# Optimization experiments

Hardware: AMD Instinct MI355X
Metric: run time of the kernel (lower is better)

## Reference

```python
import jax, jax.numpy as jnp
import numpy as np

B, X, Y, Z, C = 1, 16, 16, 16, 768
NUM_HEADS = 12


def setup_inputs() -> dict:
    key = jax.random.key(0)
    k0, k1, k2 = jax.random.split(key, 3)
    x = jax.random.normal(k0, (B, X, Y, Z, C), dtype=jnp.float32)
    # Linear weights stored as [in, out] (torch stores [out, in]; math is x @ W_in_out + b)
    w_qkv = jax.random.normal(k1, (C, 3 * C), dtype=jnp.float32) * 0.02
    b_qkv = jnp.zeros((3 * C,), dtype=jnp.float32)
    w_proj = jax.random.normal(k2, (C, C), dtype=jnp.float32) * 0.02
    b_proj = jnp.zeros((C,), dtype=jnp.float32)
    return {"x": x, "w_qkv": w_qkv, "b_qkv": b_qkv, "w_proj": w_proj, "b_proj": b_proj}


def reference(x, w_qkv, b_qkv, w_proj, b_proj):
    b, xx, yy, zz, c = x.shape
    h = NUM_HEADS
    hd = c // h
    scale = hd ** (-0.5)
    n = xx * yy * zz  # flatten 3D grid into tokens

    qkv = x.reshape(b, n, c) @ w_qkv + b_qkv          # [B, N, 3C]
    qkv = qkv.reshape(b, n, 3, h, hd).transpose(2, 0, 3, 1, 4)  # [3, B, H, N, hd]
    q, k, v = qkv[0], qkv[1], qkv[2]

    attn = jnp.einsum('bhnd,bhmd->bhnm', q * scale, k)  # [B, H, N, N]
    attn = jax.nn.softmax(attn, axis=-1)
    out = jnp.einsum('bhnm,bhmd->bhnd', attn, v)        # [B, H, N, hd]
    out = out.transpose(0, 2, 1, 3).reshape(b, n, c)
    out = out @ w_proj + b_proj
    return out.reshape(b, xx, yy, zz, c)
```

## Files before the change

### kernel.cpp

```cpp
#include <hip/hip_runtime.h>
#include <cstddef>

#define N_TOK 4096
#define C_DIM 768
#define H_NUM 12
#define C3    2304
#define NSPLIT 4

typedef unsigned short u16;
using short8  = __attribute__((ext_vector_type(8))) short;
using floatx4 = __attribute__((ext_vector_type(4))) float;
using u16x4   = __attribute__((ext_vector_type(4))) u16;
using uint4v  = __attribute__((ext_vector_type(4))) unsigned;

#define K2SCALE 0.18033688011112043f

__device__ __forceinline__ u16 f2bf(float f) {
  union { float f; unsigned u; } v; v.f = f;
  unsigned r = v.u + 0x7FFFu + ((v.u >> 16) & 1u);
  return (u16)(r >> 16);
}

__device__ __forceinline__ unsigned permpack(float a, float b) {
  union { float f; unsigned u; } x, y; x.f = a; y.f = b;
  return __builtin_amdgcn_perm(y.u, x.u, 0x07060302u);
}

__device__ __forceinline__ float aexp2(float x) {
  float r;
  asm("v_exp_f32 %0, %1" : "=v"(r) : "v"(x));
  return r;
}

__device__ __forceinline__ float arcp(float x) {
  float r;
  asm("v_rcp_f32 %0, %1" : "=v"(r) : "v"(x));
  return r;
}

__device__ __forceinline__ void pl_swap32(unsigned &a, unsigned &b) {
#if __has_builtin(__builtin_amdgcn_permlane32_swap)
  auto r = __builtin_amdgcn_permlane32_swap(a, b, false, false);
  a = r[0]; b = r[1];
#else
  asm("v_permlane32_swap_b32 %0, %1" : "+v"(a), "+v"(b));
#endif
}
__device__ __forceinline__ void pl_swap16(unsigned &a, unsigned &b) {
#if __has_builtin(__builtin_amdgcn_permlane16_swap)
  auto r = __builtin_amdgcn_permlane16_swap(a, b, false, false);
  a = r[0]; b = r[1];
#else
  asm("v_permlane16_swap_b32 %0, %1" : "+v"(a), "+v"(b));
#endif
}

__device__ __forceinline__ void gload_lds16(const void* g, void* l) {
  __builtin_amdgcn_global_load_lds(
      (const __attribute__((address_space(1))) unsigned int*)g,
      (__attribute__((address_space(3))) unsigned int*)l, 16, 0, 0);
}

__global__ void k_pre(const float* __restrict__ x, u16* __restrict__ xb,
                      const float* __restrict__ wq, u16* __restrict__ wqT,
                      const float* __restrict__ wp, u16* __restrict__ wpT,
                      float* __restrict__ Oz) {
  __shared__ float tile[32][33];
  const int b = blockIdx.x;
  if (b >= 5376) {
    size_t i = (size_t)(b - 5376) * 256 + threadIdx.x;
    float4 z; z.x = 0.f; z.y = 0.f; z.z = 0.f; z.w = 0.f;
    ((float4*)Oz)[i] = z;
    return;
  }
  if (b < 3072) {
    int i = b * 256 + threadIdx.x;
    float4 f = ((const float4*)x)[i];
    u16x4 o;
    o[0] = f2bf(f.x); o[1] = f2bf(f.y); o[2] = f2bf(f.z); o[3] = f2bf(f.w);
    ((u16x4*)xb)[i] = o;
    return;
  }
  const float* in; u16* out; int Cc, bx, by;
  if (b < 4800) { int t = b - 3072; in = wq; out = wqT; Cc = 2304; bx = t % 72; by = t / 72; }
  else          { int t = b - 4800; in = wp; out = wpT; Cc = 768;  bx = t % 24; by = t / 24; }
  const int R = 768;
  const int tx = threadIdx.x & 31;
  const int ty = threadIdx.x >> 5;
  const int c0 = bx * 32, r0 = by * 32;
#pragma unroll
  for (int i = 0; i < 32; i += 8)
    tile[ty + i][tx] = in[(size_t)(r0 + ty + i) * Cc + c0 + tx];
  __syncthreads();
#pragma unroll
  for (int i = 0; i < 32; i += 8)
    out[(size_t)(c0 + ty + i) * R + r0 + tx] = f2bf(tile[tx][ty + i]);
}

template <int MODE>
__global__ __launch_bounds__(256)
void k_gemm_bt(const u16* __restrict__ A, const u16* __restrict__ B,
               const float* __restrict__ bias, void* __restrict__ outp,
               u16* __restrict__ vT, int K) {
  __shared__ u16 As[2][128 * 32];
  __shared__ u16 Bs[2][128 * 32];
  const int tid  = threadIdx.x;
  const int wave = tid >> 6, lane = tid & 63, quad = lane >> 4, l16 = lane & 15;
  const int wrow = wave >> 1, wcol = wave & 1;
  const int bm = blockIdx.y, bn = blockIdx.x;
  const int r3 = l16 & 3;

  floatx4 acc[4][4];
#pragma unroll
  for (int i = 0; i < 4; ++i)
#pragma unroll
    for (int j = 0; j < 4; ++j)
#pragma unroll
      for (int r = 0; r < 4; ++r) acc[i][j][r] = 0.f;

  const int ar = tid >> 2;
  const int ac = ((tid & 3) ^ (ar & 3)) * 8;
  const u16* gA = A + (size_t)(bm * 128 + ar) * K + ac;
  const u16* gB = B + (size_t)(bn * 128 + ar) * K + ac;

  auto stage = [&](int b, int k0) {
    gload_lds16(gA + k0,                  &As[b][tid * 8]);
    gload_lds16(gA + k0 + (size_t)64 * K, &As[b][tid * 8 + 2048]);
    gload_lds16(gB + k0,                  &Bs[b][tid * 8]);
    gload_lds16(gB + k0 + (size_t)64 * K, &Bs[b][tid * 8 + 2048]);
  };

  stage(0, 0);
  __syncthreads();
  int buf = 0;
  for (int k0 = 0; k0 < K; k0 += 32) {
    if (k0 + 32 < K) stage(buf ^ 1, k0 + 32);
    short8 af[4], bf[4];
#pragma unroll
    for (int t = 0; t < 4; ++t) {
      af[t] = *(const short8*)&As[buf][(wrow * 64 + t * 16 + l16) * 32 + ((quad ^ r3) * 8)];
      bf[t] = *(const short8*)&Bs[buf][(wcol * 64 + t * 16 + l16) * 32 + ((quad ^ r3) * 8)];
    }
#pragma unroll
    for (int tm = 0; tm < 4; ++tm)
#pragma unroll
      for (int tn = 0; tn < 4; ++tn)
        acc[tm][tn] = __builtin_amdgcn_mfma_f32_16x16x32_bf16(af[tm], bf[tn], acc[tm][tn], 0, 0, 0);
    __syncthreads();
    buf ^= 1;
  }

  if (MODE == 0) {
    u16* qkv = (u16*)outp;
    const float qs = (bn < 6) ? K2SCALE : 1.0f;
#pragma unroll
    for (int tn = 0; tn < 4; ++tn) {
      const int col = bn * 128 + wcol * 64 + tn * 16 + l16;
      const float bc = bias[col];
      if (col < 1536) {
#pragma unroll
        for (int tm = 0; tm < 4; ++tm) {
          const int rowb = bm * 128 + wrow * 64 + tm * 16 + quad * 4;
#pragma unroll
          for (int r = 0; r < 4; ++r)
            qkv[(size_t)(rowb + r) * C3 + col] = f2bf((acc[tm][tn][r] + bc) * qs);
        }
      } else {
        const int hd_ = col - 1536;
#pragma unroll
        for (int tm = 0; tm < 4; ++tm) {
          const int rowb = bm * 128 + wrow * 64 + tm * 16 + quad * 4;
          u16x4 pk;
#pragma unroll
          for (int r = 0; r < 4; ++r) pk[r] = f2bf(acc[tm][tn][r] + bc);
          *(u16x4*)&vT[(size_t)hd_ * N_TOK + rowb] = pk;
        }
      }
    }
  } else {
    float* out = (float*)outp;
#pragma unroll
    for (int tn = 0; tn < 4; ++tn) {
      const int col = bn * 128 + wcol * 64 + tn * 16 + l16;
      const float bc = bias[col];
#pragma unroll
      for (int tm = 0; tm < 4; ++tm) {
        const int rowb = bm * 128 + wrow * 64 + tm * 16 + quad * 4;
#pragma unroll
        for (int r = 0; r < 4; ++r)
          out[(size_t)(rowb + r) * C_DIM + col] = acc[tm][tn][r] + bc;
      }
    }
  }
}

__global__ __launch_bounds__(256, 4)
void k_flash(const u16* __restrict__ qkv, const u16* __restrict__ vT,
             float* __restrict__ Opart, float* __restrict__ lpart) {
  __shared__ u16 Ks[2][64 * 64];
  __shared__ u16 Vs[2][64 * 64];
  const int tid  = threadIdx.x;
  const int wave = tid >> 6, lane = tid & 63, quad = lane >> 4, l16 = lane & 15;
  const int h = blockIdx.x >> 2, split = blockIdx.x & 3, qt = blockIdx.y;
  const int lr = tid >> 3;
  const int lc = ((tid & 7) ^ (lr & 7)) * 8;
  const int r7 = l16 & 7;
  const int kb = split * 1024;

  short8 bq[2][2];
#pragma unroll
  for (int qs = 0; qs < 2; ++qs)
#pragma unroll
    for (int ks = 0; ks < 2; ++ks)
      bq[qs][ks] = *(const short8*)&qkv[(size_t)(qt * 128 + wave * 32 + qs * 16 + l16) * C3
                                        + h * 64 + ks * 32 + quad * 8];

  const u16* gk = qkv + (size_t)lr * C3 + C_DIM + h * 64 + lc;
  const u16* gv = vT + (size_t)(h * 64 + lr) * N_TOK + lc;

  auto stage = [&](int b, int m0) {
#pragma unroll
    for (int p = 0; p < 2; ++p) {
      gload_lds16(gk + (size_t)(m0 + p * 32) * C3,    &Ks[b][p * 2048 + tid * 8]);
      gload_lds16(gv + (size_t)(p * 32) * N_TOK + m0, &Vs[b][p * 2048 + tid * 8]);
    }
  };

  floatx4 o0[4], o1[4], l0, l1, zv;
#pragma unroll
  for (int r = 0; r < 4; ++r) { zv[r] = 0.f; l0[r] = 0.f; l1[r] = 0.f; }
#pragma unroll
  for (int d = 0; d < 4; ++d)
#pragma unroll
    for (int r = 0; r < 4; ++r) { o0[d][r] = 0.f; o1[d][r] = 0.f; }

  short8 ones;
#pragma unroll
  for (int i = 0; i < 8; ++i) ones[i] = (short)0x3F80;

  auto compute = [&](int b) __attribute__((always_inline)) {
    const u16* kbp = &Ks[b][0];
    const u16* vb  = &Vs[b][0];
    floatx4 s0[4], s1[4];
    __builtin_amdgcn_s_setprio(1);
#pragma unroll
    for (int tn = 0; tn < 4; ++tn) {
      short8 ak = *(const short8*)&kbp[(tn * 16 + l16) * 64 + (quad ^ r7) * 8];
      s0[tn] = __builtin_amdgcn_mfma_f32_16x16x32_bf16(ak, bq[0][0], zv, 0, 0, 0);
      s1[tn] = __builtin_amdgcn_mfma_f32_16x16x32_bf16(ak, bq[1][0], zv, 0, 0, 0);
    }
#pragma unroll
    for (int tn = 0; tn < 4; ++tn) {
      short8 ak = *(const short8*)&kbp[(tn * 16 + l16) * 64 + ((quad + 4) ^ r7) * 8];
      s0[tn] = __builtin_amdgcn_mfma_f32_16x16x32_bf16(ak, bq[0][1], s0[tn], 0, 0, 0);
      s1[tn] = __builtin_amdgcn_mfma_f32_16x16x32_bf16(ak, bq[1][1], s1[tn], 0, 0, 0);
    }
    __builtin_amdgcn_s_setprio(0);

    unsigned pk0[4][2], pk1[4][2];
#pragma unroll
    for (int tn = 0; tn < 4; ++tn) {
      pk0[tn][0] = permpack(aexp2(s0[tn][0]), aexp2(s0[tn][1]));
      pk0[tn][1] = permpack(aexp2(s0[tn][2]), aexp2(s0[tn][3]));
      pk1[tn][0] = permpack(aexp2(s1[tn][0]), aexp2(s1[tn][1]));
      pk1[tn][1] = permpack(aexp2(s1[tn][2]), aexp2(s1[tn][3]));
    }
#pragma unroll
    for (int t1 = 0; t1 < 2; ++t1)
#pragma unroll
      for (int w = 0; w < 2; ++w) {
        pl_swap32(pk0[2 * t1][w], pk0[2 * t1 + 1][w]);
        pl_swap16(pk0[2 * t1][w], pk0[2 * t1 + 1][w]);
        pl_swap32(pk1[2 * t1][w], pk1[2 * t1 + 1][w]);
        pl_swap16(pk1[2 * t1][w], pk1[2 * t1 + 1][w]);
      }

#pragma unroll
    for (int ks = 0; ks < 2; ++ks) {
      uint4v t0v, t1v;
      t0v[0] = pk0[2 * ks][0]; t0v[1] = pk0[2 * ks][1];
      t0v[2] = pk0[2 * ks + 1][0]; t0v[3] = pk0[2 * ks + 1][1];
      t1v[0] = pk1[2 * ks][0]; t1v[1] = pk1[2 * ks][1];
      t1v[2] = pk1[2 * ks + 1][0]; t1v[3] = pk1[2 * ks + 1][1];
      const short8 ap0 = __builtin_bit_cast(short8, t0v);
      const short8 ap1 = __builtin_bit_cast(short8, t1v);
      __builtin_amdgcn_s_setprio(1);
#pragma unroll
      for (int dt = 0; dt < 4; ++dt) {
        short8 bv = *(const short8*)&vb[(dt * 16 + l16) * 64 + ((quad + 4 * ks) ^ r7) * 8];
        o0[dt] = __builtin_amdgcn_mfma_f32_16x16x32_bf16(ap0, bv, o0[dt], 0, 0, 0);
        o1[dt] = __builtin_amdgcn_mfma_f32_16x16x32_bf16(ap1, bv, o1[dt], 0, 0, 0);
      }
      l0 = __builtin_amdgcn_mfma_f32_16x16x32_bf16(ap0, ones, l0, 0, 0, 0);
      l1 = __builtin_amdgcn_mfma_f32_16x16x32_bf16(ap1, ones, l1, 0, 0, 0);
      __builtin_amdgcn_s_setprio(0);
    }
  };

  stage(0, kb);
  __syncthreads();
  int m0 = kb + 64;
  for (int it2 = 0; it2 < 7; ++it2) {
    stage(1, m0); m0 += 64;
    compute(0);
    __syncthreads();
    stage(0, m0); m0 += 64;
    compute(1);
    __syncthreads();
  }
  stage(1, m0);
  compute(0);
  __syncthreads();
  compute(1);

  const int rowg = qt * 128 + wave * 32 + quad * 4;
  float* Ob = Opart + (size_t)h * N_TOK * 64;
  float* lb = lpart + (size_t)h * N_TOK;
#pragma unroll
  for (int r = 0; r < 4; ++r) {
#pragma unroll
    for (int dt = 0; dt < 4; ++dt) {
      const int col = dt * 16 + l16;
      atomicAdd(&Ob[(size_t)(rowg + r) * 64 + col],      o0[dt][r]);
      atomicAdd(&Ob[(size_t)(rowg + 16 + r) * 64 + col], o1[dt][r]);
    }
    if (l16 == 0) {
      atomicAdd(&lb[rowg + r],      l0[r]);
      atomicAdd(&lb[rowg + 16 + r], l1[r]);
    }
  }
}

__global__ void k_combine(const float* __restrict__ Op, const float* __restrict__ lp,
                          u16* __restrict__ ao) {
  const int idx = blockIdx.x * 256 + threadIdx.x;
  const int col = idx & 63;
  const int row = idx >> 6;
  const float o = Op[(size_t)row * 64 + col];
  const float l = lp[row];
  const int h = row >> 12, q = row & 4095;
  ao[(size_t)q * C_DIM + h * 64 + col] = f2bf(o * arcp(l));
}

extern "C" void kernel_launch(void* const* d_in, const int* in_sizes, int n_in,
                              void* d_out, int out_size, void* d_ws, size_t ws_size,
                              hipStream_t stream) {
  const float* x      = (const float*)d_in[0];
  const float* w_qkv  = (const float*)d_in[1];
  const float* b_qkv  = (const float*)d_in[2];
  const float* w_proj = (const float*)d_in[3];
  const float* b_proj = (const float*)d_in[4];
  float* out = (float*)d_out;

  u16* xb     = (u16*)d_ws;
  u16* wqkvT  = xb     + (size_t)N_TOK * C_DIM;
  u16* wprojT = wqkvT  + (size_t)C3 * C_DIM;
  u16* qkv    = wprojT + (size_t)C_DIM * C_DIM;
  u16* vT     = qkv    + (size_t)N_TOK * C3;
  u16* ao     = vT     + (size_t)C_DIM * N_TOK;
  float* Opart = (float*)(ao + (size_t)N_TOK * C_DIM);
  float* lpart = Opart + (size_t)H_NUM * N_TOK * 64;

  k_pre<<<8496, 256, 0, stream>>>(x, xb, w_qkv, wqkvT, w_proj, wprojT, Opart);
  k_gemm_bt<0><<<dim3(C3 / 128, N_TOK / 128), 256, 0, stream>>>(xb, wqkvT, b_qkv, qkv, vT, C_DIM);
  k_flash<<<dim3(H_NUM * NSPLIT, N_TOK / 128), 256, 0, stream>>>(qkv, vT, Opart, lpart);
  k_combine<<<H_NUM * N_TOK * 64 / 256, 256, 0, stream>>>(Opart, lpart, ao);
  k_gemm_bt<1><<<dim3(C_DIM / 128, N_TOK / 128), 256, 0, stream>>>(ao, wprojT, b_proj, out, nullptr, C_DIM);
}
```

Before: 199.8 us.

## Process two query tiles per flash block to reuse staged K/V tiles

Each flash-attention block now holds two sets of query fragments (rows qt*128 and qt*128+2048) and runs the score and PV computation for both against every staged K/V tile. The grid's query dimension is halved, so global-to-LDS K/V traffic and barrier count per unit of work are cut in half. The cost is doubled accumulator and Q register state, which is why the launch bound drops from 4 to 3 blocks per CU. That lowers occupancy and risks register spills.

After: 216.3 us. +8.3%, slower.

```diff
diff --git a/kernel.cpp b/kernel.cpp
--- a/kernel.cpp
+++ b/kernel.cpp
@@ -194,7 +194,7 @@
   }
 }
 
-__global__ __launch_bounds__(256, 4)
+__global__ __launch_bounds__(256, 3)
 void k_flash(const u16* __restrict__ qkv, const u16* __restrict__ vT,
              float* __restrict__ Opart, float* __restrict__ lpart) {
   __shared__ u16 Ks[2][64 * 64];
@@ -207,13 +207,16 @@
   const int r7 = l16 & 7;
   const int kb = split * 1024;
 
-  short8 bq[2][2];
+  short8 bqA[2][2], bqB[2][2];
 #pragma unroll
   for (int qs = 0; qs < 2; ++qs)
 #pragma unroll
-    for (int ks = 0; ks < 2; ++ks)
-      bq[qs][ks] = *(const short8*)&qkv[(size_t)(qt * 128 + wave * 32 + qs * 16 + l16) * C3
-                                        + h * 64 + ks * 32 + quad * 8];
+    for (int ks = 0; ks < 2; ++ks) {
+      bqA[qs][ks] = *(const short8*)&qkv[(size_t)(qt * 128 + wave * 32 + qs * 16 + l16) * C3
+                                         + h * 64 + ks * 32 + quad * 8];
+      bqB[qs][ks] = *(const short8*)&qkv[(size_t)(2048 + qt * 128 + wave * 32 + qs * 16 + l16) * C3
+                                         + h * 64 + ks * 32 + quad * 8];
+    }
 
   const u16* gk = qkv + (size_t)lr * C3 + C_DIM + h * 64 + lc;
   const u16* gv = vT + (size_t)(h * 64 + lr) * N_TOK + lc;
@@ -226,19 +229,24 @@
     }
   };
 
-  floatx4 o0[4], o1[4], l0, l1, zv;
-#pragma unroll
-  for (int r = 0; r < 4; ++r) { zv[r] = 0.f; l0[r] = 0.f; l1[r] = 0.f; }
+  floatx4 oA0[4], oA1[4], oB0[4], oB1[4], lA0, lA1, lB0, lB1, zv;
+#pragma unroll
+  for (int r = 0; r < 4; ++r) {
+    zv[r] = 0.f; lA0[r] = 0.f; lA1[r] = 0.f; lB0[r] = 0.f; lB1[r] = 0.f;
+  }
 #pragma unroll
   for (int d = 0; d < 4; ++d)
 #pragma unroll
-    for (int r = 0; r < 4; ++r) { o0[d][r] = 0.f; o1[d][r] = 0.f; }
+    for (int r = 0; r < 4; ++r) {
+      oA0[d][r] = 0.f; oA1[d][r] = 0.f; oB0[d][r] = 0.f; oB1[d][r] = 0.f;
+    }
 
   short8 ones;
 #pragma unroll
   for (int i = 0; i < 8; ++i) ones[i] = (short)0x3F80;
 
-  auto compute = [&](int b) __attribute__((always_inline)) {
+  auto compute1 = [&](int b, short8 (&bq)[2][2], floatx4 (&o0)[4], floatx4 (&o1)[4],
+                      floatx4 &l0, floatx4 &l1) __attribute__((always_inline)) {
     const u16* kbp = &Ks[b][0];
     const u16* vb  = &Vs[b][0];
     floatx4 s0[4], s1[4];
@@ -295,6 +303,11 @@
       l1 = __builtin_amdgcn_mfma_f32_16x16x32_bf16(ap1, ones, l1, 0, 0, 0);
       __builtin_amdgcn_s_setprio(0);
     }
+  };
+
+  auto compute = [&](int b) __attribute__((always_inline)) {
+    compute1(b, bqA, oA0, oA1, lA0, lA1);
+    compute1(b, bqB, oB0, oB1, lB0, lB1);
   };
 
   stage(0, kb);
@@ -313,20 +326,27 @@
   __syncthreads();
   compute(1);
 
-  const int rowg = qt * 128 + wave * 32 + quad * 4;
   float* Ob = Opart + (size_t)h * N_TOK * 64;
   float* lb = lpart + (size_t)h * N_TOK;
 #pragma unroll
-  for (int r = 0; r < 4; ++r) {
-#pragma unroll
-    for (int dt = 0; dt < 4; ++dt) {
-      const int col = dt * 16 + l16;
-      atomicAdd(&Ob[(size_t)(rowg + r) * 64 + col],      o0[dt][r]);
-      atomicAdd(&Ob[(size_t)(rowg + 16 + r) * 64 + col], o1[dt][r]);
-    }
-    if (l16 == 0) {
-      atomicAdd(&lb[rowg + r],      l0[r]);
-      atomicAdd(&lb[rowg + 16 + r], l1[r]);
+  for (int qp = 0; qp < 2; ++qp) {
+    const int rowg = qp * 2048 + qt * 128 + wave * 32 + quad * 4;
+    floatx4* o0 = qp ? oB0 : oA0;
+    floatx4* o1 = qp ? oB1 : oA1;
+    floatx4& l0 = qp ? lB0 : lA0;
+    floatx4& l1 = qp ? lB1 : lA1;
+#pragma unroll
+    for (int r = 0; r < 4; ++r) {
+#pragma unroll
+      for (int dt = 0; dt < 4; ++dt) {
+        const int col = dt * 16 + l16;
+        atomicAdd(&Ob[(size_t)(rowg + r) * 64 + col],      o0[dt][r]);
+        atomicAdd(&Ob[(size_t)(rowg + 16 + r) * 64 + col], o1[dt][r]);
+      }
+      if (l16 == 0) {
+        atomicAdd(&lb[rowg + r],      l0[r]);
+        atomicAdd(&lb[rowg + 16 + r], l1[r]);
+      }
     }
   }
 }
@@ -363,7 +383,7 @@
 
   k_pre<<<8496, 256, 0, stream>>>(x, xb, w_qkv, wqkvT, w_proj, wprojT, Opart);
   k_gemm_bt<0><<<dim3(C3 / 128, N_TOK / 128), 256, 0, stream>>>(xb, wqkvT, b_qkv, qkv, vT, C_DIM);
-  k_flash<<<dim3(H_NUM * NSPLIT, N_TOK / 128), 256, 0, stream>>>(qkv, vT, Opart, lpart);
+  k_flash<<<dim3(H_NUM * NSPLIT, N_TOK / 256), 256, 0, stream>>>(qkv, vT, Opart, lpart);
   k_combine<<<H_NUM * N_TOK * 64 / 256, 256, 0, stream>>>(Opart, lpart, ao);
   k_gemm_bt<1><<<dim3(C_DIM / 128, N_TOK / 128), 256, 0, stream>>>(ao, wprojT, b_proj, out, nullptr, C_DIM);
 }
```

## Fuse split-K combine and normalization into projection GEMM A-tile staging

Applied to the files above, without the earlier changes.

Removes the separate combine kernel and the bf16 attention-output buffer. The projection GEMM now reads the fp32 partial outputs and row sums directly, normalizes and converts to bf16 while staging A tiles into LDS. It also uses 64-row M tiles, which doubles the block count. This saves one launch and a full write and read of the intermediate. In exchange, A staging becomes synchronous register loads instead of async global-to-LDS copies, and the fp32 data read per tile is wider.

After: 199.6 us. Within noise of the previous version (-0.1%).

```diff
diff --git a/kernel.cpp b/kernel.cpp
--- a/kernel.cpp
+++ b/kernel.cpp
@@ -97,13 +97,13 @@
     out[(size_t)(c0 + ty + i) * R + r0 + tx] = f2bf(tile[tx][ty + i]);
 }
 
-template <int MODE>
 __global__ __launch_bounds__(256)
-void k_gemm_bt(const u16* __restrict__ A, const u16* __restrict__ B,
-               const float* __restrict__ bias, void* __restrict__ outp,
-               u16* __restrict__ vT, int K) {
+void k_gemm_qkv(const u16* __restrict__ A, const u16* __restrict__ B,
+                const float* __restrict__ bias, u16* __restrict__ qkv,
+                u16* __restrict__ vT) {
   __shared__ u16 As[2][128 * 32];
   __shared__ u16 Bs[2][128 * 32];
+  const int K = C_DIM;
   const int tid  = threadIdx.x;
   const int wave = tid >> 6, lane = tid & 63, quad = lane >> 4, l16 = lane & 15;
   const int wrow = wave >> 1, wcol = wave & 1;
@@ -150,45 +150,28 @@
     buf ^= 1;
   }
 
-  if (MODE == 0) {
-    u16* qkv = (u16*)outp;
-    const float qs = (bn < 6) ? K2SCALE : 1.0f;
-#pragma unroll
-    for (int tn = 0; tn < 4; ++tn) {
-      const int col = bn * 128 + wcol * 64 + tn * 16 + l16;
-      const float bc = bias[col];
-      if (col < 1536) {
-#pragma unroll
-        for (int tm = 0; tm < 4; ++tm) {
-          const int rowb = bm * 128 + wrow * 64 + tm * 16 + quad * 4;
-#pragma unroll
-          for (int r = 0; r < 4; ++r)
-            qkv[(size_t)(rowb + r) * C3 + col] = f2bf((acc[tm][tn][r] + bc) * qs);
-        }
-      } else {
-        const int hd_ = col - 1536;
-#pragma unroll
-        for (int tm = 0; tm < 4; ++tm) {
-          const int rowb = bm * 128 + wrow * 64 + tm * 16 + quad * 4;
-          u16x4 pk;
-#pragma unroll
-          for (int r = 0; r < 4; ++r) pk[r] = f2bf(acc[tm][tn][r] + bc);
-          *(u16x4*)&vT[(size_t)hd_ * N_TOK + rowb] = pk;
-        }
-      }
-    }
-  } else {
-    float* out = (float*)outp;
-#pragma unroll
-    for (int tn = 0; tn < 4; ++tn) {
-      const int col = bn * 128 + wcol * 64 + tn * 16 + l16;
-      const float bc = bias[col];
+  const float qs = (bn < 6) ? K2SCALE : 1.0f;
+#pragma unroll
+  for (int tn = 0; tn < 4; ++tn) {
+    const int col = bn * 128 + wcol * 64 + tn * 16 + l16;
+    const float bc = bias[col];
+    if (col < 1536) {
 #pragma unroll
       for (int tm = 0; tm < 4; ++tm) {
         const int rowb = bm * 128 + wrow * 64 + tm * 16 + quad * 4;
 #pragma unroll
         for (int r = 0; r < 4; ++r)
-          out[(size_t)(rowb + r) * C_DIM + col] = acc[tm][tn][r] + bc;
+          qkv[(size_t)(rowb + r) * C3 + col] = f2bf((acc[tm][tn][r] + bc) * qs);
+      }
+    } else {
+      const int hd_ = col - 1536;
+#pragma unroll
+      for (int tm = 0; tm < 4; ++tm) {
+        const int rowb = bm * 128 + wrow * 64 + tm * 16 + quad * 4;
+        u16x4 pk;
+#pragma unroll
+        for (int r = 0; r < 4; ++r) pk[r] = f2bf(acc[tm][tn][r] + bc);
+        *(u16x4*)&vT[(size_t)hd_ * N_TOK + rowb] = pk;
       }
     }
   }
@@ -331,15 +314,85 @@
   }
 }
 
-__global__ void k_combine(const float* __restrict__ Op, const float* __restrict__ lp,
-                          u16* __restrict__ ao) {
-  const int idx = blockIdx.x * 256 + threadIdx.x;
-  const int col = idx & 63;
-  const int row = idx >> 6;
-  const float o = Op[(size_t)row * 64 + col];
-  const float l = lp[row];
-  const int h = row >> 12, q = row & 4095;
-  ao[(size_t)q * C_DIM + h * 64 + col] = f2bf(o * arcp(l));
+__global__ __launch_bounds__(256)
+void k_gemm_proj(const float* __restrict__ Op, const float* __restrict__ lp,
+                 const u16* __restrict__ B, const float* __restrict__ bias,
+                 float* __restrict__ out) {
+  __shared__ u16 As[2][64 * 32];
+  __shared__ u16 Bs[2][128 * 32];
+  const int K = C_DIM;
+  const int tid  = threadIdx.x;
+  const int wave = tid >> 6, lane = tid & 63, quad = lane >> 4, l16 = lane & 15;
+  const int wrow = wave >> 1, wcol = wave & 1;
+  const int bm = blockIdx.y, bn = blockIdx.x;
+  const int r3 = l16 & 3;
+
+  floatx4 acc[2][4];
+#pragma unroll
+  for (int i = 0; i < 2; ++i)
+#pragma unroll
+    for (int j = 0; j < 4; ++j)
+#pragma unroll
+      for (int r = 0; r < 4; ++r) acc[i][j][r] = 0.f;
+
+  const int ar = tid >> 2;
+  const int ac = ((tid & 3) ^ (ar & 3)) * 8;
+  const int qrow = bm * 64 + ar;
+  const u16* gB = B + (size_t)(bn * 128 + ar) * K + ac;
+
+  auto stageA = [&](int b, int k0) {
+    const int hh = k0 >> 6;
+    const float rl = arcp(lp[(size_t)hh * N_TOK + qrow]);
+    const float* src = &Op[((size_t)hh * N_TOK + qrow) * 64 + (k0 & 32) + ac];
+    float4 v0 = *(const float4*)src;
+    float4 v1 = *(const float4*)(src + 4);
+    u16x4 p0, p1;
+    p0[0] = f2bf(v0.x * rl); p0[1] = f2bf(v0.y * rl);
+    p0[2] = f2bf(v0.z * rl); p0[3] = f2bf(v0.w * rl);
+    p1[0] = f2bf(v1.x * rl); p1[1] = f2bf(v1.y * rl);
+    p1[2] = f2bf(v1.z * rl); p1[3] = f2bf(v1.w * rl);
+    *(u16x4*)&As[b][tid * 8]     = p0;
+    *(u16x4*)&As[b][tid * 8 + 4] = p1;
+  };
+  auto stageB = [&](int b, int k0) {
+    gload_lds16(gB + k0,                  &Bs[b][tid * 8]);
+    gload_lds16(gB + k0 + (size_t)64 * K, &Bs[b][tid * 8 + 2048]);
+  };
+
+  stageB(0, 0);
+  stageA(0, 0);
+  __syncthreads();
+  int buf = 0;
+  for (int k0 = 0; k0 < K; k0 += 32) {
+    if (k0 + 32 < K) { stageB(buf ^ 1, k0 + 32); stageA(buf ^ 1, k0 + 32); }
+    short8 af[2], bf[4];
+#pragma unroll
+    for (int t = 0; t < 2; ++t)
+      af[t] = *(const short8*)&As[buf][(wrow * 32 + t * 16 + l16) * 32 + ((quad ^ r3) * 8)];
+#pragma unroll
+    for (int t = 0; t < 4; ++t)
+      bf[t] = *(const short8*)&Bs[buf][(wcol * 64 + t * 16 + l16) * 32 + ((quad ^ r3) * 8)];
+#pragma unroll
+    for (int tm = 0; tm < 2; ++tm)
+#pragma unroll
+      for (int tn = 0; tn < 4; ++tn)
+        acc[tm][tn] = __builtin_amdgcn_mfma_f32_16x16x32_bf16(af[tm], bf[tn], acc[tm][tn], 0, 0, 0);
+    __syncthreads();
+    buf ^= 1;
+  }
+
+#pragma unroll
+  for (int tn = 0; tn < 4; ++tn) {
+    const int col = bn * 128 + wcol * 64 + tn * 16 + l16;
+    const float bc = bias[col];
+#pragma unroll
+    for (int tm = 0; tm < 2; ++tm) {
+      const int rowb = bm * 64 + wrow * 32 + tm * 16 + quad * 4;
+#pragma unroll
+      for (int r = 0; r < 4; ++r)
+        out[(size_t)(rowb + r) * C_DIM + col] = acc[tm][tn][r] + bc;
+    }
+  }
 }
 
 extern "C" void kernel_launch(void* const* d_in, const int* in_sizes, int n_in,
@@ -357,13 +410,11 @@
   u16* wprojT = wqkvT  + (size_t)C3 * C_DIM;
   u16* qkv    = wprojT + (size_t)C_DIM * C_DIM;
   u16* vT     = qkv    + (size_t)N_TOK * C3;
-  u16* ao     = vT     + (size_t)C_DIM * N_TOK;
-  float* Opart = (float*)(ao + (size_t)N_TOK * C_DIM);
+  float* Opart = (float*)(vT + (size_t)C_DIM * N_TOK);
   float* lpart = Opart + (size_t)H_NUM * N_TOK * 64;
 
   k_pre<<<8496, 256, 0, stream>>>(x, xb, w_qkv, wqkvT, w_proj, wprojT, Opart);
-  k_gemm_bt<0><<<dim3(C3 / 128, N_TOK / 128), 256, 0, stream>>>(xb, wqkvT, b_qkv, qkv, vT, C_DIM);
+  k_gemm_qkv<<<dim3(C3 / 128, N_TOK / 128), 256, 0, stream>>>(xb, wqkvT, b_qkv, qkv, vT);
   k_flash<<<dim3(H_NUM * NSPLIT, N_TOK / 128), 256, 0, stream>>>(qkv, vT, Opart, lpart);
-  k_combine<<<H_NUM * N_TOK * 64 / 256, 256, 0, stream>>>(Opart, lpart, ao);
-  k_gemm_bt<1><<<dim3(C_DIM / 128, N_TOK / 128), 256, 0, stream>>>(ao, wprojT, b_proj, out, nullptr, C_DIM);
-}
+  k_gemm_proj<<<dim3(C_DIM / 128, N_TOK / 64), 256, 0, stream>>>(Opart, lpart, wprojT, b_proj, out);
+}
```
